# Kernel tuning notes

Hardware: AMD Instinct MI355X
Metric: run time of the kernel (lower is better)

Reference implementation:

```python
import jax, jax.numpy as jnp
import numpy as np
import math

N_EMBD = 768
N_HEAD = 12
B, T = 4, 2048
HEAD_DIM = N_EMBD // N_HEAD


def new_gelu(x):
    # GPT-2 tanh approximation of GELU (NewGELUActivation)
    c = math.sqrt(2.0 / math.pi)
    return 0.5 * x * (1.0 + jnp.tanh(c * (x + 0.044715 * jnp.power(x, 3.0))))


def layer_norm(x, g, b, eps=1e-5):
    mu = jnp.mean(x, axis=-1, keepdims=True)
    var = jnp.mean(jnp.square(x - mu), axis=-1, keepdims=True)
    return (x - mu) * jax.lax.rsqrt(var + eps) * g + b


def setup_inputs() -> dict:
    key = jax.random.key(0)
    ks = jax.random.split(key, 12)
    s = 0.02
    return {
        "x": jax.random.normal(ks[0], (B, T, N_EMBD), dtype=jnp.float32),
        "ln1_g": jnp.ones((N_EMBD,), jnp.float32),
        "ln1_b": jnp.zeros((N_EMBD,), jnp.float32),
        "W_attn": jax.random.normal(ks[1], (N_EMBD, 3 * N_EMBD), jnp.float32) * s,
        "b_attn": jnp.zeros((3 * N_EMBD,), jnp.float32),
        "W_proj": jax.random.normal(ks[2], (N_EMBD, N_EMBD), jnp.float32) * s,
        "b_proj": jnp.zeros((N_EMBD,), jnp.float32),
        "ln2_g": jnp.ones((N_EMBD,), jnp.float32),
        "ln2_b": jnp.zeros((N_EMBD,), jnp.float32),
        "W_fc": jax.random.normal(ks[3], (N_EMBD, 4 * N_EMBD), jnp.float32) * s,
        "b_fc": jnp.zeros((4 * N_EMBD,), jnp.float32),
        "W_fc2": jax.random.normal(ks[4], (4 * N_EMBD, N_EMBD), jnp.float32) * s,
        "b_fc2": jnp.zeros((N_EMBD,), jnp.float32),
    }


def block_forward(x, ln1_g, ln1_b, W_attn, b_attn, W_proj, b_proj,
                  ln2_g, ln2_b, W_fc, b_fc, W_fc2, b_fc2):
    # ---- attention sublayer (pre-LN) ----
    h = layer_norm(x, ln1_g, ln1_b)
    qkv = h @ W_attn + b_attn                      # [B,T,3C]
    q, k, v = jnp.split(qkv, 3, axis=-1)
    q = q.reshape(B, T, N_HEAD, HEAD_DIM).transpose(0, 2, 1, 3)  # [B,H,T,D]
    k = k.reshape(B, T, N_HEAD, HEAD_DIM).transpose(0, 2, 1, 3)
    v = v.reshape(B, T, N_HEAD, HEAD_DIM).transpose(0, 2, 1, 3)
    scores = jnp.einsum('bhqd,bhkd->bhqk', q, k) / math.sqrt(HEAD_DIM)
    causal = jnp.tril(jnp.ones((T, T), dtype=bool))
    scores = jnp.where(causal[None, None, :, :], scores, -jnp.inf)
    attn = jax.nn.softmax(scores, axis=-1)
    y = jnp.einsum('bhqk,bhkd->bhqd', attn, v)      # [B,H,T,D]
    y = y.transpose(0, 2, 1, 3).reshape(B, T, N_EMBD)
    y = y @ W_proj + b_proj
    x = x + y
    # ---- MLP sublayer ----
    h = layer_norm(x, ln2_g, ln2_b)
    h = new_gelu(h @ W_fc + b_fc)
    h = h @ W_fc2 + b_fc2
    return x + h


def reference(x, ln1_g, ln1_b, W_attn, b_attn, W_proj, b_proj,
              ln2_g, ln2_b, W_fc, b_fc, W_fc2, b_fc2):
    return block_forward(x, ln1_g, ln1_b, W_attn, b_attn, W_proj, b_proj,
                         ln2_g, ln2_b, W_fc, b_fc, W_fc2, b_fc2)
```

## Files before the change

kernel.cpp:

```cpp
#include <hip/hip_runtime.h>
#include <hip/hip_bf16.h>

typedef __attribute__((ext_vector_type(8))) short short8;
typedef __attribute__((ext_vector_type(4))) float f32x4;
typedef __attribute__((ext_vector_type(8))) unsigned short u16x8;
typedef __attribute__((ext_vector_type(4))) unsigned short u16x4;

#define MFMA16(A, B, C) __builtin_amdgcn_mfma_f32_16x16x32_bf16(A, B, C, 0, 0, 0)

static __device__ __forceinline__ unsigned short f2bf(float f) {
    unsigned int u = __builtin_bit_cast(unsigned int, f);
    u += 0x7FFF + ((u >> 16) & 1);
    return (unsigned short)(u >> 16);
}

static __device__ __forceinline__ unsigned int cvt_pk_bf16(float a, float b) {
    unsigned int r;
    asm("v_cvt_pk_bf16_f32 %0, %1, %2" : "=v"(r) : "v"(a), "v"(b));
    return r;
}

typedef const __attribute__((address_space(1))) unsigned int* gas_t;
typedef __attribute__((address_space(3))) unsigned int* las_t;
static __device__ __forceinline__ void gl_lds16(const void* g, void* l) {
    __builtin_amdgcn_global_load_lds((gas_t)g, (las_t)l, 16, 0, 0);
}

__global__ void wtrans(const float* __restrict__ W, unsigned short* __restrict__ Wt,
                       int K, int N) {
    __shared__ float tl[32][33];
    const int n0 = blockIdx.x * 32, k0 = blockIdx.y * 32;
    const int tx = threadIdx.x, ty = threadIdx.y;
#pragma unroll
    for (int i = 0; i < 4; i++)
        tl[ty + 8 * i][tx] = W[(long)(k0 + ty + 8 * i) * N + n0 + tx];
    __syncthreads();
#pragma unroll
    for (int i = 0; i < 4; i++)
        Wt[(long)(n0 + ty + 8 * i) * K + k0 + tx] = f2bf(tl[tx][ty + 8 * i]);
}

__global__ __launch_bounds__(256)
void ln_fwd(const float* __restrict__ x, const float* __restrict__ gw,
            const float* __restrict__ bw, unsigned short* __restrict__ out) {
    const int row = blockIdx.x * 4 + (threadIdx.x >> 6);
    const int ln = threadIdx.x & 63;
    const float4* xr = (const float4*)(x + (long)row * 768);
    float4 v[3];
    float s = 0.f;
#pragma unroll
    for (int j = 0; j < 3; j++) {
        v[j] = xr[ln + 64 * j];
        s += v[j].x + v[j].y + v[j].z + v[j].w;
    }
#pragma unroll
    for (int off = 32; off >= 1; off >>= 1) s += __shfl_xor(s, off);
    const float mean = s * (1.0f / 768.0f);
    float sq = 0.f;
#pragma unroll
    for (int j = 0; j < 3; j++) {
        float a = v[j].x - mean, b = v[j].y - mean, c = v[j].z - mean, d = v[j].w - mean;
        sq += a * a + b * b + c * c + d * d;
    }
#pragma unroll
    for (int off = 32; off >= 1; off >>= 1) sq += __shfl_xor(sq, off);
    const float rstd = rsqrtf(sq * (1.0f / 768.0f) + 1e-5f);
#pragma unroll
    for (int j = 0; j < 3; j++) {
        const int c = ln + 64 * j;
        float4 gg = ((const float4*)gw)[c];
        float4 bb = ((const float4*)bw)[c];
        u16x4 o;
        o[0] = f2bf((v[j].x - mean) * rstd * gg.x + bb.x);
        o[1] = f2bf((v[j].y - mean) * rstd * gg.y + bb.y);
        o[2] = f2bf((v[j].z - mean) * rstd * gg.z + bb.z);
        o[3] = f2bf((v[j].w - mean) * rstd * gg.w + bb.w);
        *(u16x4*)(out + (long)row * 768 + c * 4) = o;
    }
}

template <int MODE>
__global__ __launch_bounds__(256)
void gemm_bt(const unsigned short* __restrict__ A, const unsigned short* __restrict__ Bt,
             const float* __restrict__ bias, const float* __restrict__ resid,
             void* __restrict__ Out, int M, int N, int K) {
    __shared__ unsigned short Al[128 * 64];
    __shared__ unsigned short Bl[128 * 64];
    const int tid = threadIdx.x;
    const int wv = tid >> 6, ln = tid & 63;
    const int wr = wv >> 1, wc = wv & 1;
    const int g = ln >> 4, r = ln & 15;
    const int lr = ln >> 3, l8 = ln & 7;
    const int sw = l8 ^ lr;
    const long mbase = (long)blockIdx.x * 128;
    const long nbase = (long)blockIdx.y * 128;

    f32x4 acc[4][4];
    const f32x4 zero = {0.f, 0.f, 0.f, 0.f};
#pragma unroll
    for (int m = 0; m < 4; m++)
#pragma unroll
        for (int n = 0; n < 4; n++) acc[m][n] = zero;

    const int rx = r & 7;
    for (int k0 = 0; k0 < K; k0 += 64) {
        __syncthreads();
#pragma unroll
        for (int p = 0; p < 4; p++) {
            const int row = p * 32 + wv * 8 + lr;
            gl_lds16(A + (mbase + row) * (long)K + k0 + sw * 8,
                     (char*)Al + (p * 32 + wv * 8) * 128);
            gl_lds16(Bt + (nbase + row) * (long)K + k0 + sw * 8,
                     (char*)Bl + (p * 32 + wv * 8) * 128);
        }
        __syncthreads();
#pragma unroll
        for (int ks = 0; ks < 2; ks++) {
            short8 af[4], bfr[4];
#pragma unroll
            for (int m = 0; m < 4; m++)
                af[m] = *(const short8*)(Al + (wr * 64 + m * 16 + r) * 64 + ((g + 4 * ks) ^ rx) * 8);
#pragma unroll
            for (int n = 0; n < 4; n++)
                bfr[n] = *(const short8*)(Bl + (wc * 64 + n * 16 + r) * 64 + ((g + 4 * ks) ^ rx) * 8);
#pragma unroll
            for (int m = 0; m < 4; m++)
#pragma unroll
                for (int n = 0; n < 4; n++) acc[m][n] = MFMA16(af[m], bfr[n], acc[m][n]);
        }
    }

#pragma unroll
    for (int n = 0; n < 4; n++) {
        const long col = nbase + wc * 64 + n * 16 + r;
        const float bc = bias[col];
#pragma unroll
        for (int m = 0; m < 4; m++) {
#pragma unroll
            for (int i = 0; i < 4; i++) {
                const long row = mbase + wr * 64 + m * 16 + g * 4 + i;
                float v = acc[m][n][i] + bc;
                if constexpr (MODE == 1) {
                    if (col < 768) v *= 0.18033688011112042f;
                    ((unsigned short*)Out)[row * N + col] = f2bf(v);
                } else if constexpr (MODE == 2 || MODE == 4) {
                    ((float*)Out)[row * N + col] = v + resid[row * N + col];
                } else {
                    float u = 0.7978845608028654f * (v + 0.044715f * v * v * v);
                    float gl = 0.5f * v * (1.0f + tanhf(u));
                    ((unsigned short*)Out)[row * N + col] = f2bf(gl);
                }
            }
        }
    }
}

__global__ __launch_bounds__(256)
void vtrans(const unsigned short* __restrict__ qkv, unsigned short* __restrict__ vT) {
    const int t0 = blockIdx.x * 64;
    const int bh = blockIdx.y;
    const int b = bh / 12, h = bh % 12;
    __shared__ unsigned short tl[64 * 72];
    const int tid = threadIdx.x;
#pragma unroll
    for (int p = 0; p < 2; p++) {
        int idx = p * 256 + tid;
        int row = idx >> 3, blk = idx & 7;
        int sb = (blk + row) % 9;
        *(u16x8*)(tl + row * 72 + sb * 8) =
            *(const u16x8*)(qkv + ((long)(b * 2048 + t0 + row)) * 2304 + 1536 + h * 64 + blk * 8);
    }
    __syncthreads();
#pragma unroll
    for (int p = 0; p < 2; p++) {
        int idx = p * 256 + tid;
        int d = idx >> 3, tc = (idx & 7) * 8;
        u16x8 v;
#pragma unroll
        for (int j = 0; j < 8; j++) {
            int t = tc + j;
            int sb = ((d >> 3) + t) % 9;
            v[j] = tl[t * 72 + sb * 8 + (d & 7)];
        }
        *(u16x8*)(vT + ((long)(bh * 64 + d)) * 2048 + t0 + tc) = v;
    }
}

__global__ __launch_bounds__(256)
void attn_fwd(const unsigned short* __restrict__ qkv, const unsigned short* __restrict__ vT,
              unsigned short* __restrict__ y) {
    const int pair = blockIdx.x;
    const int bh = blockIdx.y;
    const int b = bh / 12, h = bh % 12;
    __shared__ unsigned short Kl[64 * 64], Vl[64 * 64], Pl[64 * 72];
    const int tid = threadIdx.x;
    const int wv = tid >> 6, ln = tid & 63;
    const int g = ln >> 4, r = ln & 15;
    const int lr = ln >> 3, l8 = ln & 7;
    const int sw = l8 ^ lr;
    const int rx = r & 7;
    const f32x4 zero = {0.f, 0.f, 0.f, 0.f};

#pragma unroll 1
    for (int qi = 0; qi < 2; qi++) {
        const int qt = qi ? (31 - pair) : pair;
        const int q0 = qt * 64;
        const int q = wv * 16 + r;
        const long qoff = ((long)(b * 2048 + q0 + q)) * 2304 + h * 64;
        short8 bq0 = *(const short8*)(qkv + qoff + g * 8);
        short8 bq1 = *(const short8*)(qkv + qoff + 32 + g * 8);

        float mrow = -1e30f, lrow = 0.0f;
        f32x4 oacc[4];
#pragma unroll
        for (int f = 0; f < 4; f++) oacc[f] = zero;

        for (int kt = 0; kt <= qt; ++kt) {
            __syncthreads();
#pragma unroll
            for (int p = 0; p < 2; p++) {
                const int row = wv * 8 + p * 32 + lr;
                gl_lds16(qkv + ((long)(b * 2048 + kt * 64 + row)) * 2304 + 768 + h * 64 + sw * 8,
                         (char*)Kl + (wv * 8 + p * 32) * 128);
                gl_lds16(vT + ((long)(bh * 64 + row)) * 2048 + kt * 64 + sw * 8,
                         (char*)Vl + (wv * 8 + p * 32) * 128);
            }
            __syncthreads();

            f32x4 s[4];
#pragma unroll
            for (int kf = 0; kf < 4; kf++) {
                short8 a0 = *(const short8*)(Kl + (kf * 16 + r) * 64 + (g ^ rx) * 8);
                short8 a1 = *(const short8*)(Kl + (kf * 16 + r) * 64 + ((g + 4) ^ rx) * 8);
                s[kf] = MFMA16(a0, bq0, zero);
                s[kf] = MFMA16(a1, bq1, s[kf]);
            }
            if (kt == qt) {
#pragma unroll
                for (int kf = 0; kf < 4; kf++)
#pragma unroll
                    for (int i = 0; i < 4; i++)
                        if (kf * 16 + g * 4 + i > q) s[kf][i] = -1e30f;
            }
            float tmax = -1e30f;
#pragma unroll
            for (int kf = 0; kf < 4; kf++)
#pragma unroll
                for (int i = 0; i < 4; i++) tmax = fmaxf(tmax, s[kf][i]);
            tmax = fmaxf(tmax, __shfl_xor(tmax, 16));
            tmax = fmaxf(tmax, __shfl_xor(tmax, 32));
            if (__any(tmax > mrow + 6.0f)) {
                const float mnew = fmaxf(mrow, tmax);
                const float rs = __builtin_amdgcn_exp2f(mrow - mnew);
                lrow *= rs;
#pragma unroll
                for (int f = 0; f < 4; f++) oacc[f] *= rs;
                mrow = mnew;
            }
            float pv[4][4];
            float psum = 0.f;
#pragma unroll
            for (int kf = 0; kf < 4; kf++)
#pragma unroll
                for (int i = 0; i < 4; i++) {
                    pv[kf][i] = __builtin_amdgcn_exp2f(s[kf][i] - mrow);
                    psum += pv[kf][i];
                }
            psum += __shfl_xor(psum, 16);
            psum += __shfl_xor(psum, 32);
            lrow += psum;

#pragma unroll
            for (int kf = 0; kf < 4; kf++) {
                uint2 w;
                w.x = cvt_pk_bf16(pv[kf][0], pv[kf][1]);
                w.y = cvt_pk_bf16(pv[kf][2], pv[kf][3]);
                *(uint2*)(Pl + q * 72 + kf * 16 + g * 4) = w;
            }
            short8 pb0 = *(const short8*)(Pl + q * 72 + g * 8);
            short8 pb1 = *(const short8*)(Pl + q * 72 + 32 + g * 8);
#pragma unroll
            for (int f = 0; f < 4; f++) {
                short8 va0 = *(const short8*)(Vl + (f * 16 + r) * 64 + (g ^ rx) * 8);
                short8 va1 = *(const short8*)(Vl + (f * 16 + r) * 64 + ((g + 4) ^ rx) * 8);
                oacc[f] = MFMA16(va0, pb0, oacc[f]);
                oacc[f] = MFMA16(va1, pb1, oacc[f]);
            }
        }

        const float inv = 1.0f / lrow;
#pragma unroll
        for (int f = 0; f < 4; f++) {
            uint2 w;
            w.x = cvt_pk_bf16(oacc[f][0] * inv, oacc[f][1] * inv);
            w.y = cvt_pk_bf16(oacc[f][2] * inv, oacc[f][3] * inv);
            *(uint2*)(Pl + q * 72 + f * 16 + g * 4) = w;
        }
        __syncthreads();
#pragma unroll
        for (int p = 0; p < 2; p++) {
            int idx = p * 256 + tid;
            int row = idx >> 3, cc = (idx & 7) * 8;
            *(u16x8*)(y + ((long)(b * 2048 + q0 + row)) * 768 + h * 64 + cc) =
                *(const u16x8*)(Pl + row * 72 + cc);
        }
    }
}

extern "C" void kernel_launch(void* const* d_in, const int* in_sizes, int n_in,
                              void* d_out, int out_size, void* d_ws, size_t ws_size,
                              hipStream_t stream) {
    const float* x      = (const float*)d_in[0];
    const float* ln1_g  = (const float*)d_in[1];
    const float* ln1_b  = (const float*)d_in[2];
    const float* W_attn = (const float*)d_in[3];
    const float* b_attn = (const float*)d_in[4];
    const float* W_proj = (const float*)d_in[5];
    const float* b_proj = (const float*)d_in[6];
    const float* ln2_g  = (const float*)d_in[7];
    const float* ln2_b  = (const float*)d_in[8];
    const float* W_fc   = (const float*)d_in[9];
    const float* b_fc   = (const float*)d_in[10];
    const float* W_fc2  = (const float*)d_in[11];
    const float* b_fc2  = (const float*)d_in[12];

    char* ws = (char*)d_ws;
    size_t off = 0;
    auto alloc = [&](size_t bytes) -> char* {
        char* p = ws + off;
        off += (bytes + 255) & ~(size_t)255;
        return p;
    };
    unsigned short* WtA  = (unsigned short*)alloc((size_t)2304 * 768 * 2);
    unsigned short* WtP  = (unsigned short*)alloc((size_t)768 * 768 * 2);
    unsigned short* WtF  = (unsigned short*)alloc((size_t)3072 * 768 * 2);
    unsigned short* WtF2 = (unsigned short*)alloc((size_t)768 * 3072 * 2);
    unsigned short* bigA = (unsigned short*)alloc((size_t)8192 * 3072 * 2);
    float*          x1   = (float*)alloc((size_t)8192 * 768 * 4);
    unsigned short* bufD = (unsigned short*)alloc((size_t)8192 * 768 * 2);
    unsigned short* vT   = (unsigned short*)alloc((size_t)48 * 64 * 2048 * 2);

    wtrans<<<dim3(72, 24), dim3(32, 8), 0, stream>>>(W_attn, WtA, 768, 2304);
    wtrans<<<dim3(24, 24), dim3(32, 8), 0, stream>>>(W_proj, WtP, 768, 768);
    wtrans<<<dim3(96, 24), dim3(32, 8), 0, stream>>>(W_fc, WtF, 768, 3072);
    wtrans<<<dim3(24, 96), dim3(32, 8), 0, stream>>>(W_fc2, WtF2, 3072, 768);
    ln_fwd<<<2048, 256, 0, stream>>>(x, ln1_g, ln1_b, bufD);
    gemm_bt<1><<<dim3(64, 18), 256, 0, stream>>>(bufD, WtA, b_attn, nullptr, bigA, 8192, 2304, 768);
    vtrans<<<dim3(32, 48), 256, 0, stream>>>(bigA, vT);
    attn_fwd<<<dim3(16, 48), 256, 0, stream>>>(bigA, vT, bufD);
    gemm_bt<2><<<dim3(64, 6), 256, 0, stream>>>(bufD, WtP, b_proj, x, x1, 8192, 768, 768);
    ln_fwd<<<2048, 256, 0, stream>>>(x1, ln2_g, ln2_b, bufD);
    gemm_bt<3><<<dim3(64, 24), 256, 0, stream>>>(bufD, WtF, b_fc, nullptr, bigA, 8192, 3072, 768);
    gemm_bt<4><<<dim3(64, 6), 256, 0, stream>>>(bigA, WtF2, b_fc2, x1, (float*)d_out, 8192, 768, 3072);
}
```

Measured before the change: 284.9 us.

## Stage GEMM epilogue through LDS for vectorized stores and faster GELU

The GEMM epilogue now writes accumulators into shared memory one 64-row half at a time, then reads them back row-contiguously so each thread issues 16-byte bias, residual and output accesses instead of scattered scalar stores. GELU is rewritten as the equivalent sigmoid form v·sigmoid(2u) using hardware exp2 and reciprocal instead of tanhf. The bf16 conversion switches to the packed convert instruction. This adds two extra barriers and an LDS round trip per half, and the fast exp2/rcp intrinsics carry slightly lower precision than tanhf.

Result: slower. 318.3 us (+11.7%).

```diff
diff --git a/kernel.cpp b/kernel.cpp
--- a/kernel.cpp
+++ b/kernel.cpp
@@ -18,6 +18,13 @@
     unsigned int r;
     asm("v_cvt_pk_bf16_f32 %0, %1, %2" : "=v"(r) : "v"(a), "v"(b));
     return r;
+}
+
+static __device__ __forceinline__ float gelu_f(float v) {
+    const float k1 = 2.3022077646f;
+    const float k2 = 0.1029432207f;
+    float t = __builtin_amdgcn_exp2f(-(k1 * v + k2 * v * v * v));
+    return v * __builtin_amdgcn_rcpf(1.0f + t);
 }
 
 typedef const __attribute__((address_space(1))) unsigned int* gas_t;
@@ -84,8 +91,10 @@
 void gemm_bt(const unsigned short* __restrict__ A, const unsigned short* __restrict__ Bt,
              const float* __restrict__ bias, const float* __restrict__ resid,
              void* __restrict__ Out, int M, int N, int K) {
-    __shared__ unsigned short Al[128 * 64];
-    __shared__ unsigned short Bl[128 * 64];
+    __shared__ char smem[64 * 132 * 4];
+    unsigned short* Al = (unsigned short*)smem;
+    unsigned short* Bl = Al + 128 * 64;
+    float* st = (float*)smem;
     const int tid = threadIdx.x;
     const int wv = tid >> 6, ln = tid & 63;
     const int wr = wv >> 1, wc = wv & 1;
@@ -130,26 +139,58 @@
         }
     }
 
-#pragma unroll
-    for (int n = 0; n < 4; n++) {
-        const long col = nbase + wc * 64 + n * 16 + r;
-        const float bc = bias[col];
-#pragma unroll
-        for (int m = 0; m < 4; m++) {
-#pragma unroll
-            for (int i = 0; i < 4; i++) {
-                const long row = mbase + wr * 64 + m * 16 + g * 4 + i;
-                float v = acc[m][n][i] + bc;
+    const int tr = tid >> 2, seg = tid & 3;
+#pragma unroll 1
+    for (int half = 0; half < 2; half++) {
+        __syncthreads();
+        if (wr == half) {
+#pragma unroll
+            for (int m = 0; m < 4; m++)
+#pragma unroll
+                for (int n = 0; n < 4; n++)
+#pragma unroll
+                    for (int i = 0; i < 4; i++)
+                        st[(m * 16 + g * 4 + i) * 132 + wc * 64 + n * 16 + r] = acc[m][n][i];
+        }
+        __syncthreads();
+        const long row = mbase + half * 64 + tr;
+        const long cb = nbase + seg * 32;
+        if constexpr (MODE == 1 || MODE == 3) {
+            const float qs = (MODE == 1 && nbase < 768) ? 0.18033688011112042f : 1.0f;
+            unsigned short* op = (unsigned short*)Out + row * N + cb;
+#pragma unroll
+            for (int u2 = 0; u2 < 4; u2++) {
+                float4 a = *(const float4*)(st + tr * 132 + seg * 32 + u2 * 8);
+                float4 b = *(const float4*)(st + tr * 132 + seg * 32 + u2 * 8 + 4);
+                float4 ba = ((const float4*)bias)[(cb >> 2) + u2 * 2];
+                float4 bb = ((const float4*)bias)[(cb >> 2) + u2 * 2 + 1];
+                a.x += ba.x; a.y += ba.y; a.z += ba.z; a.w += ba.w;
+                b.x += bb.x; b.y += bb.y; b.z += bb.z; b.w += bb.w;
                 if constexpr (MODE == 1) {
-                    if (col < 768) v *= 0.18033688011112042f;
-                    ((unsigned short*)Out)[row * N + col] = f2bf(v);
-                } else if constexpr (MODE == 2 || MODE == 4) {
-                    ((float*)Out)[row * N + col] = v + resid[row * N + col];
+                    a.x *= qs; a.y *= qs; a.z *= qs; a.w *= qs;
+                    b.x *= qs; b.y *= qs; b.z *= qs; b.w *= qs;
                 } else {
-                    float u = 0.7978845608028654f * (v + 0.044715f * v * v * v);
-                    float gl = 0.5f * v * (1.0f + tanhf(u));
-                    ((unsigned short*)Out)[row * N + col] = f2bf(gl);
+                    a.x = gelu_f(a.x); a.y = gelu_f(a.y); a.z = gelu_f(a.z); a.w = gelu_f(a.w);
+                    b.x = gelu_f(b.x); b.y = gelu_f(b.y); b.z = gelu_f(b.z); b.w = gelu_f(b.w);
                 }
+                uint4 w;
+                w.x = cvt_pk_bf16(a.x, a.y);
+                w.y = cvt_pk_bf16(a.z, a.w);
+                w.z = cvt_pk_bf16(b.x, b.y);
+                w.w = cvt_pk_bf16(b.z, b.w);
+                *(uint4*)(op + u2 * 8) = w;
+            }
+        } else {
+            float* op = (float*)Out + row * N + cb;
+            const float* rp = resid + row * N + cb;
+#pragma unroll
+            for (int u = 0; u < 8; u++) {
+                float4 a = *(const float4*)(st + tr * 132 + seg * 32 + u * 4);
+                float4 ba = ((const float4*)bias)[(cb >> 2) + u];
+                float4 rr = ((const float4*)rp)[u];
+                a.x += ba.x + rr.x; a.y += ba.y + rr.y;
+                a.z += ba.z + rr.z; a.w += ba.w + rr.w;
+                ((float4*)op)[u] = a;
             }
         }
     }
```
